# Performance work log

Measured on AMD Instinct MI355X. Metric: run time of the kernel, lower is better.

The kernel has to match this reference:

```python
import jax, jax.numpy as jnp
import numpy as np

B, S, T = 32, 64, 64
E, H = 512, 1024   # H == 2*E required by the dot-product attention
VS, VT = 32000, 32000


def setup_inputs() -> dict:
    key = jax.random.key(0)
    ks = jax.random.split(key, 12)
    sc = 0.02
    return {
        "target_sentences": jax.random.randint(ks[0], (B, T), 0, VT),
        "target_lengths": jax.random.randint(ks[1], (B,), 1, T + 1),
        "source_lengths": jax.random.randint(ks[2], (B,), 1, S + 1),
        "source_sentences": jax.random.randint(ks[3], (B, S), 0, VS),
        "positions": jax.random.randint(ks[4], (B, S), 0, S + 1),
        "max_len": S,
        "target_len": T,
        "force": 1,
        "enc_emb": jax.random.normal(ks[5], (VS, E), jnp.float32) * sc,
        "pos_emb": jax.random.normal(ks[6], (S + 1, E), jnp.float32) * sc,
        "dec_emb": jax.random.normal(ks[7], (VT, E), jnp.float32) * sc,
        "W_h0": jax.random.normal(ks[8], (H, 2 * E), jnp.float32) * sc,
        "b_h0": jnp.zeros((H,), jnp.float32),
        "W_ih": jax.random.normal(ks[9], (4 * H, 3 * E), jnp.float32) * sc,
        "W_hh": jax.random.normal(ks[10], (4 * H, H), jnp.float32) * sc,
        "b_ih": jnp.zeros((4 * H,), jnp.float32),
        "b_hh": jnp.zeros((4 * H,), jnp.float32),
        "W_out": jax.random.normal(ks[11], (VT, 2 * E), jnp.float32) * sc,
        "b_out": jnp.zeros((VT,), jnp.float32),
    }


def reference(target_sentences, target_lengths, source_lengths, source_sentences,
              positions, max_len, target_len, force,
              enc_emb, pos_emb, dec_emb, W_h0, b_h0,
              W_ih, W_hh, b_ih, b_hh, W_out, b_out):
    # encoder: word + positional embeddings concatenated -> [B,S,2E]
    enc = jnp.concatenate([enc_emb[source_sentences], pos_emb[positions]], axis=2)
    words = dec_emb[target_sentences]                 # [B,T,E]
    h0 = jnp.mean(enc, axis=1) @ W_h0.T + b_h0        # [B,H]
    # length mask over source positions
    mask = (jnp.arange(max_len)[None, :] < source_lengths[:, None]).astype(enc.dtype)  # [B,S]

    def step(carry, w):
        h, c = carry                                  # [B,H] each
        # masked dot-product attention of decoder state against encoder outputs
        energy = jnp.einsum('bsd,bd->bs', enc, h)     # H == 2E
        attn = jax.nn.softmax(energy, axis=-1)
        masked = attn * mask
        attn_n = masked / jnp.sum(masked, axis=-1, keepdims=True)
        ctx = jnp.einsum('bs,bsd->bd', attn_n, enc)   # [B,2E]
        # LSTM cell (torch gate order i,f,g,o), teacher forcing
        x = jnp.concatenate([w, ctx], axis=-1)        # [B,3E]
        gates = x @ W_ih.T + b_ih + h @ W_hh.T + b_hh # [B,4H]
        i, f, g, o = jnp.split(gates, 4, axis=-1)
        c = jax.nn.sigmoid(f) * c + jax.nn.sigmoid(i) * jnp.tanh(g)
        h = jax.nn.sigmoid(o) * jnp.tanh(c)
        return (h, c), h

    _, hs = jax.lax.scan(step, (h0, h0), jnp.swapaxes(words, 0, 1))  # hs: [T,B,H]
    out = jnp.einsum('tbh,vh->btv', hs, W_out) + b_out               # [B,T,VT]
    return out
```

## Files before the change

### kernel.cpp

```cpp
#include <hip/hip_runtime.h>
#include <cstdint>
#include <cstddef>

#define B_  32
#define S_  64
#define T_  64
#define E_  512
#define H_  1024
#define VT_ 32000

#define AGENT __HIP_MEMORY_SCOPE_AGENT

using short8  = __attribute__((ext_vector_type(8))) short;
using floatx4 = __attribute__((ext_vector_type(4))) float;
using us4     = __attribute__((ext_vector_type(4))) unsigned short;
using u64x2   = __attribute__((ext_vector_type(2))) unsigned long long;

__device__ __forceinline__ unsigned short f2bf(float f) {
  unsigned int u = __builtin_bit_cast(unsigned int, f);
  u = u + 0x7fffu + ((u >> 16) & 1u);
  return (unsigned short)(u >> 16);
}
__device__ __forceinline__ float sigf(float x) { return 1.f / (1.f + __expf(-x)); }

__device__ __forceinline__ short8 aload16(const unsigned short* p) {
  u64x2 v;
  v[0] = __hip_atomic_load((unsigned long long*)p,       __ATOMIC_RELAXED, AGENT);
  v[1] = __hip_atomic_load((unsigned long long*)(p + 4), __ATOMIC_RELAXED, AGENT);
  return __builtin_bit_cast(short8, v);
}
__device__ __forceinline__ float4 aload16f(const float* p) {
  u64x2 v;
  v[0] = __hip_atomic_load((unsigned long long*)p,       __ATOMIC_RELAXED, AGENT);
  v[1] = __hip_atomic_load((unsigned long long*)(p + 2), __ATOMIC_RELAXED, AGENT);
  return __builtin_bit_cast(float4, v);
}
__device__ __forceinline__ void astore8(unsigned short* p, us4 v) {
  __hip_atomic_store((unsigned long long*)p, __builtin_bit_cast(unsigned long long, v),
                     __ATOMIC_RELAXED, AGENT);
}
__device__ __forceinline__ void astoref(float* p, float v) {
  __hip_atomic_store((unsigned int*)p, __builtin_bit_cast(unsigned int, v),
                     __ATOMIC_RELAXED, AGENT);
}

__device__ __forceinline__ void glds16(const void* g, void* l) {
  __builtin_amdgcn_global_load_lds(
      (const __attribute__((address_space(1))) unsigned int*)g,
      (__attribute__((address_space(3))) unsigned int*)l, 16, 0, 0);
}

__device__ __forceinline__ void gridbar(unsigned int* bar, unsigned int step) {
  asm volatile("s_waitcnt vmcnt(0)" ::: "memory");
  __syncthreads();
  if (threadIdx.x == 0) {
    const unsigned g = blockIdx.x & 7u;
    unsigned prev = __hip_atomic_fetch_add(&bar[g * 16], 1u, __ATOMIC_RELAXED, AGENT);
    if ((prev & 31u) == 31u) {
      unsigned rp = __hip_atomic_fetch_add(&bar[128], 1u, __ATOMIC_RELAXED, AGENT);
      if ((rp & 7u) == 7u)
        __hip_atomic_store(&bar[144], (rp >> 3) + 1u, __ATOMIC_RELAXED, AGENT);
    }
    while (__hip_atomic_load(&bar[144], __ATOMIC_RELAXED, AGENT) < step + 1u)
      __builtin_amdgcn_s_sleep(4);
    asm volatile("" ::: "memory");
  }
  __syncthreads();
}

__global__ void build_enc(const int* __restrict__ ss, const int* __restrict__ pp,
                          const float* __restrict__ enc_emb, const float* __restrict__ pos_emb,
                          float* __restrict__ enc) {
  int row = blockIdx.x, tid = threadIdx.x;
  int tok = ss[row], pos = pp[row];
  float2 a = *(const float2*)&enc_emb[(size_t)tok * E_ + tid * 2];
  float2 p = *(const float2*)&pos_emb[(size_t)pos * E_ + tid * 2];
  *(float2*)&enc[(size_t)row * 1024 + tid * 2]       = a;
  *(float2*)&enc[(size_t)row * 1024 + 512 + tid * 2] = p;
}

__global__ void enc_mean(const float* __restrict__ enc, float* __restrict__ em) {
  int b = blockIdx.x, tid = threadIdx.x;
  float4 acc = {0, 0, 0, 0};
  for (int s = 0; s < S_; ++s) {
    float4 v = *(const float4*)&enc[((size_t)b * S_ + s) * 1024 + tid * 4];
    acc.x += v.x; acc.y += v.y; acc.z += v.z; acc.w += v.w;
  }
  const float inv = 1.f / 64.f;
  acc.x *= inv; acc.y *= inv; acc.z *= inv; acc.w *= inv;
  *(float4*)&em[(size_t)b * 1024 + tid * 4] = acc;
}

__global__ __launch_bounds__(256) void h0_kernel(
    const float* __restrict__ em, const float* __restrict__ W_h0, const float* __restrict__ b_h0,
    float* __restrict__ hbuf, float* __restrict__ cbuf, unsigned short* __restrict__ xbuf) {
  int o = blockIdx.x * 4 + (threadIdx.x >> 6);
  int l = threadIdx.x & 63;
  int b = o >> 10, j = o & 1023;
  const float* wr = &W_h0[(size_t)j * 1024];
  const float* ev = &em[(size_t)b * 1024];
  float v = 0.f;
  #pragma unroll
  for (int i = 0; i < 16; ++i) v += wr[l + i * 64] * ev[l + i * 64];
  #pragma unroll
  for (int off = 32; off; off >>= 1) v += __shfl_down(v, off);
  if (l == 0) {
    v += b_h0[j];
    hbuf[b * 1024 + j] = v;
    cbuf[b * 1024 + j] = v;
    xbuf[b * 2048 + 1024 + j] = f2bf(v);
  }
}

__global__ void build_words(const int* __restrict__ ts, const float* __restrict__ dec_emb,
                            unsigned short* __restrict__ words_bf) {
  int bi = blockIdx.x;
  int b = bi >> 6, t = bi & 63;
  int tok = ts[bi];
  int m = t * 32 + b;
  int tid = threadIdx.x;
  float2 v = *(const float2*)&dec_emb[(size_t)tok * E_ + tid * 2];
  words_bf[(size_t)m * E_ + tid * 2]     = f2bf(v.x);
  words_bf[(size_t)m * E_ + tid * 2 + 1] = f2bf(v.y);
}

__global__ void cast_wstep(const float* __restrict__ W_ih, const float* __restrict__ W_hh,
                           unsigned short* __restrict__ Wstep) {
  int r = blockIdx.x, c = threadIdx.x * 4;
  float4 a = *(const float4*)&W_ih[(size_t)r * 1536 + 512 + c];
  float4 h = *(const float4*)&W_hh[(size_t)r * 1024 + c];
  us4 va; va[0] = f2bf(a.x); va[1] = f2bf(a.y); va[2] = f2bf(a.z); va[3] = f2bf(a.w);
  us4 vh; vh[0] = f2bf(h.x); vh[1] = f2bf(h.y); vh[2] = f2bf(h.z); vh[3] = f2bf(h.w);
  *(us4*)&Wstep[(size_t)r * 2048 + c]        = va;
  *(us4*)&Wstep[(size_t)r * 2048 + 1024 + c] = vh;
}

__global__ void cast_wout(const float* __restrict__ W, unsigned short* __restrict__ Wb) {
  size_t i = ((size_t)blockIdx.x * 256 + threadIdx.x) * 4;
  float4 f = *(const float4*)&W[i];
  us4 v; v[0] = f2bf(f.x); v[1] = f2bf(f.y); v[2] = f2bf(f.z); v[3] = f2bf(f.w);
  *(us4*)&Wb[i] = v;
}

__global__ __launch_bounds__(256) void gemm_bb(
    const unsigned short* __restrict__ A, int lda,
    const void* __restrict__ Bv, int ldb, int bfmt,
    float* __restrict__ C, int ldc,
    const float* __restrict__ bias1, const float* __restrict__ bias2,
    int K, int mode) {
  __shared__ unsigned short sA[128 * 64];
  __shared__ unsigned short sB[128 * 64];
  const int tid = threadIdx.x;
  const int nwg  = gridDim.x * gridDim.y;
  const int flat = blockIdx.y * gridDim.x + blockIdx.x;
  const int u    = (flat & 7) * (nwg >> 3) + (flat >> 3);
  const int by   = u % gridDim.y;
  const int bx   = u / gridDim.y;
  const int n0 = bx * 128, m0 = by * 128;
  const int w = tid >> 6, l = tid & 63;
  const int wm = w >> 1, wn = w & 1;
  const int l15 = l & 15, q = l >> 4;
  const int xs = (l15 & 7) << 3;
  const int gr = l >> 3;
  const int gk = (l & 7) << 3;

  floatx4 acc[4][4];
  #pragma unroll
  for (int i = 0; i < 4; ++i)
    #pragma unroll
    for (int j = 0; j < 4; ++j) acc[i][j] = (floatx4){0.f, 0.f, 0.f, 0.f};

  for (int k0 = 0; k0 < K; k0 += 64) {
    __syncthreads();
    #pragma unroll
    for (int p = 0; p < 4; ++p) {
      int inst = w * 4 + p;
      int row = inst * 8 + gr;
      int kk = gk ^ ((row & 7) << 3);
      glds16(&A[(size_t)(m0 + row) * lda + k0 + kk], &sA[inst * 512]);
    }
    if (bfmt) {
      const unsigned short* Bw = (const unsigned short*)Bv;
      #pragma unroll
      for (int p = 0; p < 4; ++p) {
        int inst = w * 4 + p;
        int row = inst * 8 + gr;
        int kk = gk ^ ((row & 7) << 3);
        glds16(&Bw[(size_t)(n0 + row) * ldb + k0 + kk], &sB[inst * 512]);
      }
    } else {
      const float* Bw = (const float*)Bv;
      #pragma unroll
      for (int p = 0; p < 8; ++p) {
        int idx4 = p * 256 + tid;
        int row = idx4 >> 4, kc = (idx4 & 15) << 2;
        float4 f = *(const float4*)&Bw[(size_t)(n0 + row) * ldb + k0 + kc];
        us4 v; v[0] = f2bf(f.x); v[1] = f2bf(f.y); v[2] = f2bf(f.z); v[3] = f2bf(f.w);
        *(us4*)&sB[row * 64 + (kc ^ ((row & 7) << 3))] = v;
      }
    }
    __syncthreads();
    #pragma unroll
    for (int kk2 = 0; kk2 < 2; ++kk2) {
      const int kr = (kk2 * 32 + q * 8) ^ xs;
      short8 af[4], bf8[4];
      #pragma unroll
      for (int mt = 0; mt < 4; ++mt)
        af[mt] = *(short8*)&sA[(wm * 64 + mt * 16 + l15) * 64 + kr];
      #pragma unroll
      for (int nt = 0; nt < 4; ++nt)
        bf8[nt] = *(short8*)&sB[(wn * 64 + nt * 16 + l15) * 64 + kr];
      #pragma unroll
      for (int mt = 0; mt < 4; ++mt)
        #pragma unroll
        for (int nt = 0; nt < 4; ++nt)
          acc[mt][nt] = __builtin_amdgcn_mfma_f32_16x16x32_bf16(af[mt], bf8[nt], acc[mt][nt], 0, 0, 0);
    }
  }

  #pragma unroll
  for (int mt = 0; mt < 4; ++mt)
    #pragma unroll
    for (int nt = 0; nt < 4; ++nt)
      #pragma unroll
      for (int r = 0; r < 4; ++r) {
        int m = m0 + wm * 64 + mt * 16 + q * 4 + r;
        int n = n0 + wn * 64 + nt * 16 + l15;
        float v = acc[mt][nt][r];
        if (bias1) v += bias1[n];
        if (bias2) v += bias2[n];
        if (mode == 0) {
          C[(size_t)m * ldc + n] = v;
        } else {
          int b = m & 31, t = m >> 5;
          C[(size_t)(b * 64 + t) * ldc + n] = v;
        }
      }
}

__global__ __launch_bounds__(256, 1) void recurrence(
    const float* __restrict__ enc, float* __restrict__ hbuf, float* __restrict__ cbuf,
    unsigned short* __restrict__ xb0, unsigned short* __restrict__ xb1,
    const unsigned short* __restrict__ Wstep, const float* __restrict__ gw,
    unsigned short* __restrict__ hs, const int* __restrict__ slen,
    unsigned int* __restrict__ bar) {
  __shared__ unsigned short wlds[16 * 2048];
  __shared__ float red[2048];

  const int tid = threadIdx.x;
  const int w = tid >> 6, l = tid & 63;
  const int l15 = l & 15, q = l >> 4;
  const int u0 = blockIdx.x * 4;

  #pragma unroll
  for (int ii = 0; ii < 16; ++ii) {
    int idx = ii * 256 + tid;
    int n = idx >> 8;
    int kc = (idx & 255) << 3;
    int rn = (n >> 2) * 1024 + u0 + (n & 3);
    short8 v = *(const short8*)&Wstep[(size_t)rn * 2048 + kc];
    *(short8*)&wlds[n * 2048 + (kc ^ ((n & 7) << 3))] = v;
  }

  const int lenb = (blockIdx.x < 32) ? slen[blockIdx.x] : 0;
  float* hsh  = red;
  float* esh  = red + 1024;
  float* ashp = red + 1088;

  unsigned int bt = 0;

  for (int t = 0; t < 64; ++t) {
    unsigned short* xc = (t & 1) ? xb1 : xb0;
    unsigned short* xn = (t & 1) ? xb0 : xb1;

    if (blockIdx.x < 32) {
      int b = blockIdx.x;
      *(float4*)&hsh[tid * 4] = aload16f(&hbuf[(size_t)b * 1024 + tid * 4]);
      __syncthreads();
      for (int si = 0; si < 16; ++si) {
        int s = w * 16 + si;
        const float* er = &enc[((size_t)b * S_ + s) * 1024];
        float v = 0.f;
        #pragma unroll
        for (int i = 0; i < 16; ++i) v += er[l + i * 64] * hsh[l + i * 64];
        #pragma unroll
        for (int off = 32; off; off >>= 1) v += __shfl_down(v, off);
        if (l == 0) esh[s] = v;
      }
      __syncthreads();
      if (tid < 64) {
        float e = (tid < lenb) ? esh[tid] : -1e30f;
        float m = e;
        #pragma unroll
        for (int off = 32; off; off >>= 1) m = fmaxf(m, __shfl_down(m, off));
        m = __shfl(m, 0);
        float p = (tid < lenb) ? __expf(e - m) : 0.f;
        float s = p;
        #pragma unroll
        for (int off = 32; off; off >>= 1) s += __shfl_down(s, off);
        s = __shfl(s, 0);
        ashp[tid] = p / s;
      }
      __syncthreads();
      float4 acc = {0, 0, 0, 0};
      const float* eb = &enc[(size_t)b * S_ * 1024 + tid * 4];
      for (int s = 0; s < S_; ++s) {
        float a = ashp[s];
        float4 ev = *(const float4*)&eb[(size_t)s * 1024];
        acc.x += a * ev.x; acc.y += a * ev.y; acc.z += a * ev.z; acc.w += a * ev.w;
      }
      us4 v; v[0] = f2bf(acc.x); v[1] = f2bf(acc.y); v[2] = f2bf(acc.z); v[3] = f2bf(acc.w);
      astore8(&xc[b * 2048 + tid * 4], v);
    }
    gridbar(bar, bt); ++bt;

    {
      floatx4 acc0 = (floatx4){0.f, 0.f, 0.f, 0.f};
      floatx4 acc1 = (floatx4){0.f, 0.f, 0.f, 0.f};
      const int kbase = w * 512;
      #pragma unroll 8
      for (int ks = 0; ks < 16; ++ks) {
        int k0 = kbase + ks * 32 + q * 8;
        short8 b8 = *(short8*)&wlds[l15 * 2048 + (k0 ^ ((l15 & 7) << 3))];
        short8 a0 = aload16(&xc[(size_t)l15 * 2048 + k0]);
        short8 a1 = aload16(&xc[(size_t)(16 + l15) * 2048 + k0]);
        acc0 = __builtin_amdgcn_mfma_f32_16x16x32_bf16(a0, b8, acc0, 0, 0, 0);
        acc1 = __builtin_amdgcn_mfma_f32_16x16x32_bf16(a1, b8, acc1, 0, 0, 0);
      }
      #pragma unroll
      for (int r = 0; r < 4; ++r) {
        red[w * 512 + (q * 4 + r) * 16 + l15]      = acc0[r];
        red[w * 512 + (16 + q * 4 + r) * 16 + l15] = acc1[r];
      }
      __syncthreads();
      if (tid < 128) {
        int b = tid >> 2, ui = tid & 3;
        float g4[4];
        #pragma unroll
        for (int g = 0; g < 4; ++g) {
          int n = g * 4 + ui;
          float s = red[b * 16 + n] + red[512 + b * 16 + n] +
                    red[1024 + b * 16 + n] + red[1536 + b * 16 + n];
          s += gw[(size_t)(t * 32 + b) * 4096 + g * 1024 + u0 + ui];
          g4[g] = s;
        }
        int u = u0 + ui;
        float c_old = cbuf[b * 1024 + u];
        float fi = sigf(g4[0]);
        float ff = sigf(g4[1]);
        float gg = tanhf(g4[2]);
        float fo = sigf(g4[3]);
        float cn = ff * c_old + fi * gg;
        float hn = fo * tanhf(cn);
        cbuf[b * 1024 + u] = cn;
        astoref(&hbuf[b * 1024 + u], hn);
        unsigned short hb = f2bf(hn);
        hs[(size_t)(t * 32 + b) * 1024 + u] = hb;
        unsigned hv = (unsigned)hb;
        unsigned p0 = __shfl(hv, (l & ~3) + 0);
        unsigned p1 = __shfl(hv, (l & ~3) + 1);
        unsigned p2 = __shfl(hv, (l & ~3) + 2);
        unsigned p3 = __shfl(hv, (l & ~3) + 3);
        if (ui == 0) {
          unsigned long long pk = (unsigned long long)p0 |
                                  ((unsigned long long)p1 << 16) |
                                  ((unsigned long long)p2 << 32) |
                                  ((unsigned long long)p3 << 48);
          __hip_atomic_store((unsigned long long*)&xn[b * 2048 + 1024 + u0], pk,
                             __ATOMIC_RELAXED, AGENT);
        }
      }
    }
    gridbar(bar, bt); ++bt;
  }
}

extern "C" void kernel_launch(void* const* d_in, const int* in_sizes, int n_in,
                              void* d_out, int out_size, void* d_ws, size_t ws_size,
                              hipStream_t stream) {
  const int*   ts     = (const int*)d_in[0];
  const int*   slen   = (const int*)d_in[2];
  const int*   ss     = (const int*)d_in[3];
  const int*   pp     = (const int*)d_in[4];
  const float* enc_emb = (const float*)d_in[8];
  const float* pos_emb = (const float*)d_in[9];
  const float* dec_emb = (const float*)d_in[10];
  const float* W_h0   = (const float*)d_in[11];
  const float* b_h0   = (const float*)d_in[12];
  const float* W_ih   = (const float*)d_in[13];
  const float* W_hh   = (const float*)d_in[14];
  const float* b_ih   = (const float*)d_in[15];
  const float* b_hh   = (const float*)d_in[16];
  const float* W_out  = (const float*)d_in[17];
  const float* b_out  = (const float*)d_in[18];
  float* out = (float*)d_out;

  char* base = (char*)d_ws;
  size_t off = 0;
  auto carve = [&](size_t bytes) { void* p = base + off; off += (bytes + 255) & ~(size_t)255; return p; };
  float*          enc      = (float*)carve((size_t)B_ * S_ * 1024 * 4);
  float*          em       = (float*)carve((size_t)B_ * 1024 * 4);
  float*          hbuf     = (float*)carve((size_t)B_ * 1024 * 4);
  float*          cbuf     = (float*)carve((size_t)B_ * 1024 * 4);
  unsigned short* xb0      = (unsigned short*)carve((size_t)B_ * 2048 * 2);
  unsigned short* xb1      = (unsigned short*)carve((size_t)B_ * 2048 * 2);
  unsigned short* words_bf = (unsigned short*)carve((size_t)2048 * E_ * 2);
  unsigned short* Wstep    = (unsigned short*)carve((size_t)4096 * 2048 * 2);
  float*          gw       = (float*)carve((size_t)2048 * 4096 * 4);
  unsigned short* hs       = (unsigned short*)carve((size_t)2048 * 1024 * 2);
  unsigned int*   bar      = (unsigned int*)carve(1024);
  unsigned short* Wob      = (unsigned short*)carve((size_t)VT_ * 1024 * 2);
  const bool haveWob = (off <= ws_size);

  hipMemsetAsync(bar, 0, 1024, stream);

  build_enc  <<<B_ * S_, 256, 0, stream>>>(ss, pp, enc_emb, pos_emb, enc);
  enc_mean   <<<B_,      256, 0, stream>>>(enc, em);
  h0_kernel  <<<(B_ * H_) / 4, 256, 0, stream>>>(em, W_h0, b_h0, hbuf, cbuf, xb0);
  build_words<<<B_ * T_, 256, 0, stream>>>(ts, dec_emb, words_bf);
  cast_wstep <<<4096,    256, 0, stream>>>(W_ih, W_hh, Wstep);
  if (haveWob) cast_wout<<<VT_, 256, 0, stream>>>(W_out, Wob);

  gemm_bb<<<dim3(4096 / 128, 2048 / 128), 256, 0, stream>>>(
      words_bf, E_, (const void*)W_ih, 1536, 0, gw, 4096, b_ih, b_hh, E_, 0);

  recurrence<<<256, 256, 0, stream>>>(enc, hbuf, cbuf, xb0, xb1, Wstep, gw, hs, slen, bar);

  gemm_bb<<<dim3(VT_ / 128, 2048 / 128), 256, 0, stream>>>(
      hs, H_, haveWob ? (const void*)Wob : (const void*)W_out, H_, haveWob ? 1 : 0,
      out, VT_, b_out, nullptr, H_, 1);
}
```

Measured before the change: 2.285 ms.

## Rework recurrence sync with per-block slot barrier and per-step ring buffers

Replaces the hierarchical atomic-counter grid barrier with per-block arrival slots that one wavefront polls, and replaces the double-buffered x/h state with per-timestep ring buffers placed in the output buffer. This lets plain loads stand in for atomic loads. It also stores the encoder in bf16 for the attention dot products, keeps the LSTM cell state in registers, prefetches the input-gate contributions before the barrier, interleaves the block-to-unit mapping, and skips the last barrier. The aim is to cut per-step synchronization latency and memory traffic in the sequential loop, at the cost of bf16 attention precision. The scratch ring buffers in the output region are assumed to be overwritten later by the final GEMM.

After: 2.190 ms. -4.1%, faster.

```diff
diff --git a/kernel.cpp b/kernel.cpp
--- a/kernel.cpp
+++ b/kernel.cpp
@@ -14,27 +14,18 @@
 using short8  = __attribute__((ext_vector_type(8))) short;
 using floatx4 = __attribute__((ext_vector_type(4))) float;
 using us4     = __attribute__((ext_vector_type(4))) unsigned short;
-using u64x2   = __attribute__((ext_vector_type(2))) unsigned long long;
 
 __device__ __forceinline__ unsigned short f2bf(float f) {
   unsigned int u = __builtin_bit_cast(unsigned int, f);
   u = u + 0x7fffu + ((u >> 16) & 1u);
   return (unsigned short)(u >> 16);
 }
+__device__ __forceinline__ float bf2f(short s) {
+  unsigned int u = ((unsigned int)(unsigned short)s) << 16;
+  return __builtin_bit_cast(float, u);
+}
 __device__ __forceinline__ float sigf(float x) { return 1.f / (1.f + __expf(-x)); }
 
-__device__ __forceinline__ short8 aload16(const unsigned short* p) {
-  u64x2 v;
-  v[0] = __hip_atomic_load((unsigned long long*)p,       __ATOMIC_RELAXED, AGENT);
-  v[1] = __hip_atomic_load((unsigned long long*)(p + 4), __ATOMIC_RELAXED, AGENT);
-  return __builtin_bit_cast(short8, v);
-}
-__device__ __forceinline__ float4 aload16f(const float* p) {
-  u64x2 v;
-  v[0] = __hip_atomic_load((unsigned long long*)p,       __ATOMIC_RELAXED, AGENT);
-  v[1] = __hip_atomic_load((unsigned long long*)(p + 2), __ATOMIC_RELAXED, AGENT);
-  return __builtin_bit_cast(float4, v);
-}
 __device__ __forceinline__ void astore8(unsigned short* p, us4 v) {
   __hip_atomic_store((unsigned long long*)p, __builtin_bit_cast(unsigned long long, v),
                      __ATOMIC_RELAXED, AGENT);
@@ -50,33 +41,38 @@
       (__attribute__((address_space(3))) unsigned int*)l, 16, 0, 0);
 }
 
-__device__ __forceinline__ void gridbar(unsigned int* bar, unsigned int step) {
+__device__ __forceinline__ void gridbar(unsigned int* slots, unsigned int arrive) {
   asm volatile("s_waitcnt vmcnt(0)" ::: "memory");
   __syncthreads();
-  if (threadIdx.x == 0) {
-    const unsigned g = blockIdx.x & 7u;
-    unsigned prev = __hip_atomic_fetch_add(&bar[g * 16], 1u, __ATOMIC_RELAXED, AGENT);
-    if ((prev & 31u) == 31u) {
-      unsigned rp = __hip_atomic_fetch_add(&bar[128], 1u, __ATOMIC_RELAXED, AGENT);
-      if ((rp & 7u) == 7u)
-        __hip_atomic_store(&bar[144], (rp >> 3) + 1u, __ATOMIC_RELAXED, AGENT);
-    }
-    while (__hip_atomic_load(&bar[144], __ATOMIC_RELAXED, AGENT) < step + 1u)
-      __builtin_amdgcn_s_sleep(4);
-    asm volatile("" ::: "memory");
+  if (threadIdx.x < 64) {
+    if (threadIdx.x == 0)
+      __hip_atomic_store(&slots[blockIdx.x], arrive, __ATOMIC_RELAXED, AGENT);
+    const int l = threadIdx.x;
+    for (;;) {
+      unsigned a0 = __hip_atomic_load(&slots[l],       __ATOMIC_RELAXED, AGENT);
+      unsigned a1 = __hip_atomic_load(&slots[l + 64],  __ATOMIC_RELAXED, AGENT);
+      unsigned a2 = __hip_atomic_load(&slots[l + 128], __ATOMIC_RELAXED, AGENT);
+      unsigned a3 = __hip_atomic_load(&slots[l + 192], __ATOMIC_RELAXED, AGENT);
+      if (__all(a0 >= arrive && a1 >= arrive && a2 >= arrive && a3 >= arrive)) break;
+      __builtin_amdgcn_s_sleep(1);
+    }
   }
   __syncthreads();
 }
 
 __global__ void build_enc(const int* __restrict__ ss, const int* __restrict__ pp,
                           const float* __restrict__ enc_emb, const float* __restrict__ pos_emb,
-                          float* __restrict__ enc) {
+                          float* __restrict__ enc, unsigned short* __restrict__ enc_bf) {
   int row = blockIdx.x, tid = threadIdx.x;
   int tok = ss[row], pos = pp[row];
   float2 a = *(const float2*)&enc_emb[(size_t)tok * E_ + tid * 2];
   float2 p = *(const float2*)&pos_emb[(size_t)pos * E_ + tid * 2];
   *(float2*)&enc[(size_t)row * 1024 + tid * 2]       = a;
   *(float2*)&enc[(size_t)row * 1024 + 512 + tid * 2] = p;
+  unsigned pa = (unsigned)f2bf(a.x) | ((unsigned)f2bf(a.y) << 16);
+  unsigned pb = (unsigned)f2bf(p.x) | ((unsigned)f2bf(p.y) << 16);
+  *(unsigned*)&enc_bf[(size_t)row * 1024 + tid * 2]       = pa;
+  *(unsigned*)&enc_bf[(size_t)row * 1024 + 512 + tid * 2] = pb;
 }
 
 __global__ void enc_mean(const float* __restrict__ enc, float* __restrict__ em) {
@@ -93,7 +89,7 @@
 
 __global__ __launch_bounds__(256) void h0_kernel(
     const float* __restrict__ em, const float* __restrict__ W_h0, const float* __restrict__ b_h0,
-    float* __restrict__ hbuf, float* __restrict__ cbuf, unsigned short* __restrict__ xbuf) {
+    float* __restrict__ cbuf, float* __restrict__ hr0, unsigned short* __restrict__ xr0) {
   int o = blockIdx.x * 4 + (threadIdx.x >> 6);
   int l = threadIdx.x & 63;
   int b = o >> 10, j = o & 1023;
@@ -106,9 +102,9 @@
   for (int off = 32; off; off >>= 1) v += __shfl_down(v, off);
   if (l == 0) {
     v += b_h0[j];
-    hbuf[b * 1024 + j] = v;
     cbuf[b * 1024 + j] = v;
-    xbuf[b * 2048 + 1024 + j] = f2bf(v);
+    hr0[b * 1024 + j] = v;
+    xr0[b * 2048 + 1024 + j] = f2bf(v);
   }
 }
 
@@ -239,18 +235,20 @@
 }
 
 __global__ __launch_bounds__(256, 1) void recurrence(
-    const float* __restrict__ enc, float* __restrict__ hbuf, float* __restrict__ cbuf,
-    unsigned short* __restrict__ xb0, unsigned short* __restrict__ xb1,
+    const unsigned short* __restrict__ enc_bf, float* __restrict__ cbuf,
+    unsigned short* __restrict__ xring, float* __restrict__ hring,
     const unsigned short* __restrict__ Wstep, const float* __restrict__ gw,
     unsigned short* __restrict__ hs, const int* __restrict__ slen,
-    unsigned int* __restrict__ bar) {
+    unsigned int* __restrict__ slots) {
   __shared__ unsigned short wlds[16 * 2048];
   __shared__ float red[2048];
+  __shared__ float esh[64];
+  __shared__ float ashp[64];
 
   const int tid = threadIdx.x;
   const int w = tid >> 6, l = tid & 63;
   const int l15 = l & 15, q = l >> 4;
-  const int u0 = blockIdx.x * 4;
+  const int u0 = (((blockIdx.x & 7) << 5) | (blockIdx.x >> 3)) << 2;
 
   #pragma unroll
   for (int ii = 0; ii < 16; ++ii) {
@@ -263,26 +261,41 @@
   }
 
   const int lenb = (blockIdx.x < 32) ? slen[blockIdx.x] : 0;
-  float* hsh  = red;
-  float* esh  = red + 1024;
-  float* ashp = red + 1088;
-
-  unsigned int bt = 0;
+  float creg = (tid < 128) ? cbuf[(tid >> 2) * 1024 + u0 + (tid & 3)] : 0.f;
 
   for (int t = 0; t < 64; ++t) {
-    unsigned short* xc = (t & 1) ? xb1 : xb0;
-    unsigned short* xn = (t & 1) ? xb0 : xb1;
+    const unsigned short* xc = xring + (size_t)t * 65536;
+    unsigned short*       xn = xring + (size_t)(t + 1) * 65536;
+    const float*        hcur = hring + (size_t)t * 32768;
+    float*               hnx = hring + (size_t)(t + 1) * 32768;
+
+    float gp0 = 0.f, gp1 = 0.f, gp2 = 0.f, gp3 = 0.f;
+    if (tid < 128) {
+      const float* gp = &gw[(size_t)(t * 32 + (tid >> 2)) * 4096 + u0 + (tid & 3)];
+      gp0 = gp[0]; gp1 = gp[1024]; gp2 = gp[2048]; gp3 = gp[3072];
+    }
 
     if (blockIdx.x < 32) {
-      int b = blockIdx.x;
-      *(float4*)&hsh[tid * 4] = aload16f(&hbuf[(size_t)b * 1024 + tid * 4]);
-      __syncthreads();
+      const int b = blockIdx.x;
+      const float* hb = &hcur[b * 1024];
+      float4 h0v = *(const float4*)&hb[l * 8];
+      float4 h1v = *(const float4*)&hb[l * 8 + 4];
+      float4 h2v = *(const float4*)&hb[512 + l * 8];
+      float4 h3v = *(const float4*)&hb[512 + l * 8 + 4];
+      const unsigned short* ebase = &enc_bf[(size_t)b * 65536];
       for (int si = 0; si < 16; ++si) {
         int s = w * 16 + si;
-        const float* er = &enc[((size_t)b * S_ + s) * 1024];
-        float v = 0.f;
-        #pragma unroll
-        for (int i = 0; i < 16; ++i) v += er[l + i * 64] * hsh[l + i * 64];
+        const unsigned short* er = ebase + (size_t)s * 1024;
+        short8 e0 = *(const short8*)&er[l * 8];
+        short8 e1 = *(const short8*)&er[512 + l * 8];
+        float v = bf2f(e0[0]) * h0v.x + bf2f(e0[1]) * h0v.y +
+                  bf2f(e0[2]) * h0v.z + bf2f(e0[3]) * h0v.w +
+                  bf2f(e0[4]) * h1v.x + bf2f(e0[5]) * h1v.y +
+                  bf2f(e0[6]) * h1v.z + bf2f(e0[7]) * h1v.w +
+                  bf2f(e1[0]) * h2v.x + bf2f(e1[1]) * h2v.y +
+                  bf2f(e1[2]) * h2v.z + bf2f(e1[3]) * h2v.w +
+                  bf2f(e1[4]) * h3v.x + bf2f(e1[5]) * h3v.y +
+                  bf2f(e1[6]) * h3v.z + bf2f(e1[7]) * h3v.w;
         #pragma unroll
         for (int off = 32; off; off >>= 1) v += __shfl_down(v, off);
         if (l == 0) esh[s] = v;
@@ -303,27 +316,29 @@
       }
       __syncthreads();
       float4 acc = {0, 0, 0, 0};
-      const float* eb = &enc[(size_t)b * S_ * 1024 + tid * 4];
-      for (int s = 0; s < S_; ++s) {
+      const unsigned short* eb = &enc_bf[(size_t)b * 65536 + tid * 4];
+      #pragma unroll 8
+      for (int s = 0; s < 64; ++s) {
         float a = ashp[s];
-        float4 ev = *(const float4*)&eb[(size_t)s * 1024];
-        acc.x += a * ev.x; acc.y += a * ev.y; acc.z += a * ev.z; acc.w += a * ev.w;
+        us4 ev = *(const us4*)&eb[(size_t)s * 1024];
+        acc.x += a * bf2f((short)ev[0]); acc.y += a * bf2f((short)ev[1]);
+        acc.z += a * bf2f((short)ev[2]); acc.w += a * bf2f((short)ev[3]);
       }
       us4 v; v[0] = f2bf(acc.x); v[1] = f2bf(acc.y); v[2] = f2bf(acc.z); v[3] = f2bf(acc.w);
-      astore8(&xc[b * 2048 + tid * 4], v);
-    }
-    gridbar(bar, bt); ++bt;
+      astore8((unsigned short*)&xc[b * 2048 + tid * 4], v);
+    }
+    gridbar(slots, (unsigned)(2 * t + 1));
 
     {
       floatx4 acc0 = (floatx4){0.f, 0.f, 0.f, 0.f};
       floatx4 acc1 = (floatx4){0.f, 0.f, 0.f, 0.f};
       const int kbase = w * 512;
-      #pragma unroll 8
+      #pragma unroll
       for (int ks = 0; ks < 16; ++ks) {
         int k0 = kbase + ks * 32 + q * 8;
         short8 b8 = *(short8*)&wlds[l15 * 2048 + (k0 ^ ((l15 & 7) << 3))];
-        short8 a0 = aload16(&xc[(size_t)l15 * 2048 + k0]);
-        short8 a1 = aload16(&xc[(size_t)(16 + l15) * 2048 + k0]);
+        short8 a0 = *(const short8*)&xc[(size_t)l15 * 2048 + k0];
+        short8 a1 = *(const short8*)&xc[(size_t)(16 + l15) * 2048 + k0];
         acc0 = __builtin_amdgcn_mfma_f32_16x16x32_bf16(a0, b8, acc0, 0, 0, 0);
         acc1 = __builtin_amdgcn_mfma_f32_16x16x32_bf16(a1, b8, acc1, 0, 0, 0);
       }
@@ -334,29 +349,27 @@
       }
       __syncthreads();
       if (tid < 128) {
-        int b = tid >> 2, ui = tid & 3;
+        int bb = tid >> 2, ui = tid & 3;
+        int uu = u0 + ui;
         float g4[4];
         #pragma unroll
         for (int g = 0; g < 4; ++g) {
           int n = g * 4 + ui;
-          float s = red[b * 16 + n] + red[512 + b * 16 + n] +
-                    red[1024 + b * 16 + n] + red[1536 + b * 16 + n];
-          s += gw[(size_t)(t * 32 + b) * 4096 + g * 1024 + u0 + ui];
-          g4[g] = s;
+          g4[g] = red[bb * 16 + n] + red[512 + bb * 16 + n] +
+                  red[1024 + bb * 16 + n] + red[1536 + bb * 16 + n];
         }
-        int u = u0 + ui;
-        float c_old = cbuf[b * 1024 + u];
+        g4[0] += gp0; g4[1] += gp1; g4[2] += gp2; g4[3] += gp3;
         float fi = sigf(g4[0]);
         float ff = sigf(g4[1]);
         float gg = tanhf(g4[2]);
         float fo = sigf(g4[3]);
-        float cn = ff * c_old + fi * gg;
+        float cn = ff * creg + fi * gg;
+        creg = cn;
         float hn = fo * tanhf(cn);
-        cbuf[b * 1024 + u] = cn;
-        astoref(&hbuf[b * 1024 + u], hn);
-        unsigned short hb = f2bf(hn);
-        hs[(size_t)(t * 32 + b) * 1024 + u] = hb;
-        unsigned hv = (unsigned)hb;
+        astoref(&hnx[bb * 1024 + uu], hn);
+        unsigned short hb16 = f2bf(hn);
+        hs[(size_t)(t * 32 + bb) * 1024 + uu] = hb16;
+        unsigned hv = (unsigned)hb16;
         unsigned p0 = __shfl(hv, (l & ~3) + 0);
         unsigned p1 = __shfl(hv, (l & ~3) + 1);
         unsigned p2 = __shfl(hv, (l & ~3) + 2);
@@ -366,12 +379,12 @@
                                   ((unsigned long long)p1 << 16) |
                                   ((unsigned long long)p2 << 32) |
                                   ((unsigned long long)p3 << 48);
-          __hip_atomic_store((unsigned long long*)&xn[b * 2048 + 1024 + u0], pk,
+          __hip_atomic_store((unsigned long long*)&xn[bb * 2048 + 1024 + u0], pk,
                              __ATOMIC_RELAXED, AGENT);
         }
       }
     }
-    gridbar(bar, bt); ++bt;
+    if (t != 63) gridbar(slots, (unsigned)(2 * t + 2));
   }
 }
 
@@ -400,10 +413,7 @@
   auto carve = [&](size_t bytes) { void* p = base + off; off += (bytes + 255) & ~(size_t)255; return p; };
   float*          enc      = (float*)carve((size_t)B_ * S_ * 1024 * 4);
   float*          em       = (float*)carve((size_t)B_ * 1024 * 4);
-  float*          hbuf     = (float*)carve((size_t)B_ * 1024 * 4);
   float*          cbuf     = (float*)carve((size_t)B_ * 1024 * 4);
-  unsigned short* xb0      = (unsigned short*)carve((size_t)B_ * 2048 * 2);
-  unsigned short* xb1      = (unsigned short*)carve((size_t)B_ * 2048 * 2);
   unsigned short* words_bf = (unsigned short*)carve((size_t)2048 * E_ * 2);
   unsigned short* Wstep    = (unsigned short*)carve((size_t)4096 * 2048 * 2);
   float*          gw       = (float*)carve((size_t)2048 * 4096 * 4);
@@ -412,11 +422,16 @@
   unsigned short* Wob      = (unsigned short*)carve((size_t)VT_ * 1024 * 2);
   const bool haveWob = (off <= ws_size);
 
+  char* ob = (char*)d_out;
+  unsigned short* enc_bf = (unsigned short*)(ob);
+  unsigned short* xring  = (unsigned short*)(ob + 4194304);
+  float*          hring  = (float*)(ob + 4194304 + 8519680);
+
   hipMemsetAsync(bar, 0, 1024, stream);
 
-  build_enc  <<<B_ * S_, 256, 0, stream>>>(ss, pp, enc_emb, pos_emb, enc);
+  build_enc  <<<B_ * S_, 256, 0, stream>>>(ss, pp, enc_emb, pos_emb, enc, enc_bf);
   enc_mean   <<<B_,      256, 0, stream>>>(enc, em);
-  h0_kernel  <<<(B_ * H_) / 4, 256, 0, stream>>>(em, W_h0, b_h0, hbuf, cbuf, xb0);
+  h0_kernel  <<<(B_ * H_) / 4, 256, 0, stream>>>(em, W_h0, b_h0, cbuf, hring, xring);
   build_words<<<B_ * T_, 256, 0, stream>>>(ts, dec_emb, words_bf);
   cast_wstep <<<4096,    256, 0, stream>>>(W_ih, W_hh, Wstep);
   if (haveWob) cast_wout<<<VT_, 256, 0, stream>>>(W_out, Wob);
@@ -424,7 +439,7 @@
   gemm_bb<<<dim3(4096 / 128, 2048 / 128), 256, 0, stream>>>(
       words_bf, E_, (const void*)W_ih, 1536, 0, gw, 4096, b_ih, b_hh, E_, 0);
 
-  recurrence<<<256, 256, 0, stream>>>(enc, hbuf, cbuf, xb0, xb1, Wstep, gw, hs, slen, bar);
+  recurrence<<<256, 256, 0, stream>>>(enc_bf, cbuf, xring, hring, Wstep, gw, hs, slen, bar);
 
   gemm_bb<<<dim3(VT_ / 128, 2048 / 128), 256, 0, stream>>>(
       hs, H_, haveWob ? (const void*)Wob : (const void*)W_out, H_, haveWob ? 1 : 0,
```
